# Kernel tuning notes

Hardware: AMD Instinct MI355X
Metric: run time of the kernel (lower is better)

## Reference

```python
import jax, jax.numpy as jnp
import numpy as np

K = 256            # number of learned permutations (config['k'])
N = 256            # nb_experts
NOISE_FACTOR = 0.01
TAU_INITIAL = 1e-3
TAU_FINAL = 1e-7
N_ITERS_MIN, N_ITERS_MAX = 20, 150
ITERS_TOTAL = 100 * 1000   # epochs_for_learning_permutation * steps_per_epoch
EPS = 1e-20


def setup_inputs() -> dict:
    key = jax.random.key(0)
    k1, k2 = jax.random.split(key)
    # keras RandomUniform initializer default range is [-0.05, 0.05]
    plw = jax.random.uniform(k1, (K, N, N), jnp.float32, minval=-0.05, maxval=0.05)
    u = jax.random.uniform(k2, (K, N, N), jnp.float32)
    return {"permutation_log_weights": plw, "u": u, "iterations": 5000}


def reference(permutation_log_weights, u, iterations):
    # Linear-in-log10 interpolation of tau and linear interpolation of n_iters
    # over the learning schedule (tfp.math.interp_regular_1d_grid with clamping).
    frac = min(max(float(iterations) / ITERS_TOTAL, 0.0), 1.0)
    log_tau = np.log10(TAU_INITIAL) + frac * (np.log10(TAU_FINAL) - np.log10(TAU_INITIAL))
    tau = np.float32(10.0 ** log_tau)
    n_iters = int(N_ITERS_MIN + frac * (N_ITERS_MAX - N_ITERS_MIN))

    # Gumbel noise from uniform samples, scaled, then temperature scaling.
    noise = -jnp.log(-jnp.log(u + EPS) + EPS) * jnp.float32(NOISE_FACTOR)
    log_alpha = (permutation_log_weights + noise) / tau  # [K, N, N]

    # Log-domain Sinkhorn: alternate row / column log-normalization.
    def step(la, _):
        la = la - jax.scipy.special.logsumexp(la, axis=2, keepdims=True)
        la = la - jax.scipy.special.logsumexp(la, axis=1, keepdims=True)
        return la, None

    log_alpha, _ = jax.lax.scan(step, log_alpha, None, length=n_iters)
    return jnp.exp(log_alpha)  # [K, N, N] near-doubly-stochastic
```

## Files before the change

kernel.cpp:

```cpp
#include <hip/hip_runtime.h>


#define KMAT 256

typedef unsigned uint2_ev __attribute__((ext_vector_type(2)));

__device__ __forceinline__ float fast_exp2(float x) {
#if __has_builtin(__builtin_amdgcn_exp2f)
  return __builtin_amdgcn_exp2f(x);
#else
  return exp2f(x);
#endif
}

__device__ __forceinline__ float fast_log2(float x) {
#if __has_builtin(__builtin_amdgcn_logf)
  return __builtin_amdgcn_logf(x);
#else
  return __log2f(x);
#endif
}

__device__ __forceinline__ float fast_rcp(float x) {
#if __has_builtin(__builtin_amdgcn_rcpf)
  return __builtin_amdgcn_rcpf(x);
#else
  return 1.0f / x;
#endif
}

__device__ __forceinline__ float2 pk_fma(float2 a, float2 b, float2 c) {
  float2 d;
  asm("v_pk_fma_f32 %0, %1, %2, %3" : "=v"(d) : "v"(a), "v"(b), "v"(c));
  return d;
}
__device__ __forceinline__ float2 pk_mul(float2 a, float2 b) {
  float2 d;
  asm("v_pk_mul_f32 %0, %1, %2" : "=v"(d) : "v"(a), "v"(b));
  return d;
}
__device__ __forceinline__ float2 pk_add(float2 a, float2 b) {
  float2 d;
  asm("v_pk_add_f32 %0, %1, %2" : "=v"(d) : "v"(a), "v"(b));
  return d;
}
__device__ __forceinline__ float2 pk_sub1(float2 a, float s) {
  return make_float2(a.x - s, a.y - s);
}

template <int CTRL>
__device__ __forceinline__ float dpp_movf(float x) {
  return __int_as_float(
      __builtin_amdgcn_update_dpp(0, __float_as_int(x), CTRL, 0xf, 0xf, true));
}

__device__ __forceinline__ float hgroup_max(float x) {
  x = fmaxf(x, dpp_movf<0x121>(x));
  x = fmaxf(x, dpp_movf<0x122>(x));
  x = fmaxf(x, dpp_movf<0x124>(x));
  x = fmaxf(x, dpp_movf<0x128>(x));
#if __has_builtin(__builtin_amdgcn_permlane16_swap)
  uint2_ev r = __builtin_amdgcn_permlane16_swap(
      (unsigned)__float_as_int(x), (unsigned)__float_as_int(x), false, false);
  return fmaxf(__int_as_float((int)r.x), __int_as_float((int)r.y));
#else
  return fmaxf(x, __shfl_xor(x, 16, 64));
#endif
}

__device__ __forceinline__ float hgroup_sum(float x) {
  x += dpp_movf<0x121>(x);
  x += dpp_movf<0x122>(x);
  x += dpp_movf<0x124>(x);
  x += dpp_movf<0x128>(x);
#if __has_builtin(__builtin_amdgcn_permlane16_swap)
  uint2_ev r = __builtin_amdgcn_permlane16_swap(
      (unsigned)__float_as_int(x), (unsigned)__float_as_int(x), false, false);
  return __int_as_float((int)r.x) + __int_as_float((int)r.y);
#else
  return x + __shfl_xor(x, 16, 64);
#endif
}

__device__ __forceinline__ float x32_max(float x) {
#if __has_builtin(__builtin_amdgcn_permlane32_swap)
  uint2_ev r = __builtin_amdgcn_permlane32_swap(
      (unsigned)__float_as_int(x), (unsigned)__float_as_int(x), false, false);
  return fmaxf(__int_as_float((int)r.x), __int_as_float((int)r.y));
#else
  return fmaxf(x, __shfl_xor(x, 32, 64));
#endif
}

__device__ __forceinline__ float x32_sum(float x) {
#if __has_builtin(__builtin_amdgcn_permlane32_swap)
  uint2_ev r = __builtin_amdgcn_permlane32_swap(
      (unsigned)__float_as_int(x), (unsigned)__float_as_int(x), false, false);
  return __int_as_float((int)r.x) + __int_as_float((int)r.y);
#else
  return x + __shfl_xor(x, 32, 64);
#endif
}

__device__ __forceinline__ float gumbel_la(float p, float uv, float scale) {
  float lnu = fast_log2(uv + 1e-20f) * 0.69314718056f;
  float g = fast_log2(1e-20f - lnu) * (-0.0069314718056f);
  return (p + g) * scale;
}

__global__ __launch_bounds__(1024, 4) void lp_sinkhorn_kernel(
    const float* __restrict__ plw, const float* __restrict__ uin,
    const int* __restrict__ itp, float* __restrict__ out) {
  const int k = blockIdx.x;
  const int t = threadIdx.x;
  const int br = t >> 5;
  const int bc = t & 31;
  const int wv = t >> 6;
  const int lane = t & 63;

  __shared__ float red[16 * 256];
  __shared__ float colv[256];

  double frac = (double)itp[0] * 1e-5;
  frac = frac < 0.0 ? 0.0 : (frac > 1.0 ? 1.0 : frac);
  const int n_iters = (int)(20.0 + frac * 130.0);
  const float tauf = (float)exp2((-3.0 - 4.0 * frac) * 3.3219280948873623);
  const float scale = (float)(1.4426950408889634 / (double)tauf);

  float2 la[8][4];

  const float4* p4 = (const float4*)plw + k * 16384;
  const float4* u4 = (const float4*)uin + k * 16384;
#pragma unroll
  for (int i = 0; i < 8; ++i) {
    const int ridx = ((br << 3) + i) * 64 + (bc << 1);
    float4 p0 = p4[ridx];
    float4 p1 = p4[ridx + 1];
    float4 v0 = u4[ridx];
    float4 v1 = u4[ridx + 1];
    la[i][0] = make_float2(gumbel_la(p0.x, v0.x, scale),
                           gumbel_la(p0.y, v0.y, scale));
    la[i][1] = make_float2(gumbel_la(p0.z, v0.z, scale),
                           gumbel_la(p0.w, v0.w, scale));
    la[i][2] = make_float2(gumbel_la(p1.x, v1.x, scale),
                           gumbel_la(p1.y, v1.y, scale));
    la[i][3] = make_float2(gumbel_la(p1.z, v1.z, scale),
                           gumbel_la(p1.w, v1.w, scale));
  }

  const int jlo = (lane < 32) ? 0 : 4;

#pragma unroll
  for (int i = 0; i < 8; ++i) {
    float m = fmaxf(la[i][0].x, la[i][0].y);
#pragma unroll
    for (int p = 1; p < 4; ++p) m = fmaxf(m, fmaxf(la[i][p].x, la[i][p].y));
    m = hgroup_max(m);
    float s = 0.f;
#pragma unroll
    for (int p = 0; p < 4; ++p)
      s += fast_exp2(la[i][p].x - m) + fast_exp2(la[i][p].y - m);
    s = hgroup_sum(s);
    const float lse = m + fast_log2(s);
#pragma unroll
    for (int p = 0; p < 4; ++p) la[i][p] = pk_sub1(la[i][p], lse);
  }

  {
    float cm[8];
#pragma unroll
    for (int p = 0; p < 4; ++p) {
      float2 m = la[0][p];
#pragma unroll
      for (int i = 1; i < 8; ++i)
        m = make_float2(fmaxf(m.x, la[i][p].x), fmaxf(m.y, la[i][p].y));
      cm[2 * p] = x32_max(m.x);
      cm[2 * p + 1] = x32_max(m.y);
    }
#pragma unroll
    for (int j = 0; j < 4; ++j) red[wv * 256 + bc + 32 * (jlo + j)] = cm[jlo + j];
    __syncthreads();

    float keepm = 0.f;
    if (t < 256) {
      float v = red[t];
#pragma unroll
      for (int w = 1; w < 16; ++w) v = fmaxf(v, red[w * 256 + t]);
      keepm = v;
      colv[t] = v;
    }
    __syncthreads();

    float cs[8];
#pragma unroll
    for (int p = 0; p < 4; ++p) {
      const float2 mj = make_float2(colv[bc + 32 * (2 * p)],
                                    colv[bc + 32 * (2 * p + 1)]);
      float2 s = make_float2(0.f, 0.f);
#pragma unroll
      for (int i = 0; i < 8; ++i)
        s = make_float2(s.x + fast_exp2(la[i][p].x - mj.x),
                        s.y + fast_exp2(la[i][p].y - mj.y));
      cs[2 * p] = x32_sum(s.x);
      cs[2 * p + 1] = x32_sum(s.y);
    }
    __syncthreads();
#pragma unroll
    for (int j = 0; j < 4; ++j) red[wv * 256 + bc + 32 * (jlo + j)] = cs[jlo + j];
    __syncthreads();

    if (t < 256) {
      float v = red[t];
#pragma unroll
      for (int w = 1; w < 16; ++w) v += red[w * 256 + t];
      colv[t] = keepm + fast_log2(v);
    }
    __syncthreads();

#pragma unroll
    for (int p = 0; p < 4; ++p) {
      const float2 lse = make_float2(colv[bc + 32 * (2 * p)],
                                     colv[bc + 32 * (2 * p + 1)]);
#pragma unroll
      for (int i = 0; i < 8; ++i)
        la[i][p] = make_float2(fast_exp2(la[i][p].x - lse.x),
                               fast_exp2(la[i][p].y - lse.y));
    }
  }

  float uo[8] = {1.f, 1.f, 1.f, 1.f, 1.f, 1.f, 1.f, 1.f};
  float2 v2[4] = {make_float2(1.f, 1.f), make_float2(1.f, 1.f),
                  make_float2(1.f, 1.f), make_float2(1.f, 1.f)};

  for (int iter = 1; iter < n_iters; ++iter) {
#pragma unroll
    for (int i = 0; i < 8; ++i) {
      float2 a0 = pk_mul(la[i][0], v2[0]);
      float2 a1 = pk_mul(la[i][1], v2[1]);
      a0 = pk_fma(la[i][2], v2[2], a0);
      a1 = pk_fma(la[i][3], v2[3], a1);
      a0 = pk_add(a0, a1);
      const float s = hgroup_sum(a0.x + a0.y);
      uo[i] = fast_rcp(s);
    }

    float2 cs2[4] = {make_float2(0.f, 0.f), make_float2(0.f, 0.f),
                     make_float2(0.f, 0.f), make_float2(0.f, 0.f)};
#pragma unroll
    for (int i = 0; i < 8; ++i) {
      const float2 ub = make_float2(uo[i], uo[i]);
#pragma unroll
      for (int p = 0; p < 4; ++p) cs2[p] = pk_fma(la[i][p], ub, cs2[p]);
    }
    float cs[8];
#pragma unroll
    for (int p = 0; p < 4; ++p) {
      cs[2 * p] = x32_sum(cs2[p].x);
      cs[2 * p + 1] = x32_sum(cs2[p].y);
    }
#pragma unroll
    for (int j = 0; j < 4; ++j) red[wv * 256 + bc + 32 * (jlo + j)] = cs[jlo + j];
    __syncthreads();

    if (t < 128) {
      const float2* r2 = (const float2*)red;
      float2 v = r2[t];
#pragma unroll
      for (int w = 1; w < 16; ++w) v = pk_add(v, r2[w * 128 + t]);
      float2* c2 = (float2*)colv;
      c2[t] = make_float2(fast_rcp(v.x), fast_rcp(v.y));
    }
    __syncthreads();

#pragma unroll
    for (int p = 0; p < 4; ++p)
      v2[p] = make_float2(colv[bc + 32 * (2 * p)],
                          colv[bc + 32 * (2 * p + 1)]);
  }

  float4* o4 = (float4*)out + k * 16384;
#pragma unroll
  for (int i = 0; i < 8; ++i) {
    const int ridx = ((br << 3) + i) * 64 + (bc << 1);
    const float2 ub = make_float2(uo[i], uo[i]);
    float2 r0 = pk_mul(pk_mul(la[i][0], ub), v2[0]);
    float2 r1 = pk_mul(pk_mul(la[i][1], ub), v2[1]);
    float2 r2 = pk_mul(pk_mul(la[i][2], ub), v2[2]);
    float2 r3 = pk_mul(pk_mul(la[i][3], ub), v2[3]);
    float4 a, b;
    a.x = r0.x; a.y = r0.y; a.z = r1.x; a.w = r1.y;
    b.x = r2.x; b.y = r2.y; b.z = r3.x; b.w = r3.y;
    o4[ridx] = a;
    o4[ridx + 1] = b;
  }
}

extern "C" void kernel_launch(void* const* d_in, const int* in_sizes, int n_in,
                              void* d_out, int out_size, void* d_ws,
                              size_t ws_size, hipStream_t stream) {
  const float* plw = (const float*)d_in[0];
  const float* u = (const float*)d_in[1];
  const int* iters = (const int*)d_in[2];
  float* out = (float*)d_out;
  (void)in_sizes; (void)n_in; (void)out_size; (void)d_ws; (void)ws_size;
  lp_sinkhorn_kernel<<<dim3(KMAT), dim3(1024), 0, stream>>>(plw, u, iters, out);
}
```

Before: 99.97 us.

## Replace cross-half permlane32 column reduction with padded LDS all-thread reduction

Column partial sums and maxes are no longer combined across wave halves with permlane32 swaps. Every thread now writes its per-column partials into a larger padded LDS buffer, one row per 32-thread group. All 1024 threads then reduce it, four lanes per column, finishing with DPP quad shuffles instead of 128 or 256 threads doing serial 16-way loops. The inline-asm packed FP32 helpers are replaced with scalar float code the compiler can schedule, and the launch bounds move to an explicit waves-per-EU attribute. The aim is a shorter critical path in the per-iteration column reduction, at the cost of more LDS traffic and possibly losing packed-math issue.

```diff
diff --git a/kernel.cpp b/kernel.cpp
--- a/kernel.cpp
+++ b/kernel.cpp
@@ -2,6 +2,7 @@
 
 
 #define KMAT 256
+#define RSTRIDE 264
 
 typedef unsigned uint2_ev __attribute__((ext_vector_type(2)));
 
@@ -27,25 +28,6 @@
 #else
   return 1.0f / x;
 #endif
-}
-
-__device__ __forceinline__ float2 pk_fma(float2 a, float2 b, float2 c) {
-  float2 d;
-  asm("v_pk_fma_f32 %0, %1, %2, %3" : "=v"(d) : "v"(a), "v"(b), "v"(c));
-  return d;
-}
-__device__ __forceinline__ float2 pk_mul(float2 a, float2 b) {
-  float2 d;
-  asm("v_pk_mul_f32 %0, %1, %2" : "=v"(d) : "v"(a), "v"(b));
-  return d;
-}
-__device__ __forceinline__ float2 pk_add(float2 a, float2 b) {
-  float2 d;
-  asm("v_pk_add_f32 %0, %1, %2" : "=v"(d) : "v"(a), "v"(b));
-  return d;
-}
-__device__ __forceinline__ float2 pk_sub1(float2 a, float s) {
-  return make_float2(a.x - s, a.y - s);
 }
 
 template <int CTRL>
@@ -82,33 +64,15 @@
 #endif
 }
 
-__device__ __forceinline__ float x32_max(float x) {
-#if __has_builtin(__builtin_amdgcn_permlane32_swap)
-  uint2_ev r = __builtin_amdgcn_permlane32_swap(
-      (unsigned)__float_as_int(x), (unsigned)__float_as_int(x), false, false);
-  return fmaxf(__int_as_float((int)r.x), __int_as_float((int)r.y));
-#else
-  return fmaxf(x, __shfl_xor(x, 32, 64));
-#endif
-}
-
-__device__ __forceinline__ float x32_sum(float x) {
-#if __has_builtin(__builtin_amdgcn_permlane32_swap)
-  uint2_ev r = __builtin_amdgcn_permlane32_swap(
-      (unsigned)__float_as_int(x), (unsigned)__float_as_int(x), false, false);
-  return __int_as_float((int)r.x) + __int_as_float((int)r.y);
-#else
-  return x + __shfl_xor(x, 32, 64);
-#endif
-}
-
 __device__ __forceinline__ float gumbel_la(float p, float uv, float scale) {
   float lnu = fast_log2(uv + 1e-20f) * 0.69314718056f;
   float g = fast_log2(1e-20f - lnu) * (-0.0069314718056f);
   return (p + g) * scale;
 }
 
-__global__ __launch_bounds__(1024, 4) void lp_sinkhorn_kernel(
+__global__ __launch_bounds__(1024)
+__attribute__((amdgpu_waves_per_eu(4, 4)))
+void lp_sinkhorn_kernel(
     const float* __restrict__ plw, const float* __restrict__ uin,
     const int* __restrict__ itp, float* __restrict__ out) {
   const int k = blockIdx.x;
@@ -118,8 +82,12 @@
   const int wv = t >> 6;
   const int lane = t & 63;
 
-  __shared__ float red[16 * 256];
+  __shared__ float red[32 * RSTRIDE];
   __shared__ float colv[256];
+
+  const int rbase = br * RSTRIDE + bc;
+  const int slot = 16 * wv + (lane >> 2);
+  const int q = lane & 3;
 
   double frac = (double)itp[0] * 1e-5;
   frac = frac < 0.0 ? 0.0 : (frac > 1.0 ? 1.0 : frac);
@@ -148,8 +116,6 @@
                            gumbel_la(p1.w, v1.w, scale));
   }
 
-  const int jlo = (lane < 32) ? 0 : 4;
-
 #pragma unroll
   for (int i = 0; i < 8; ++i) {
     float m = fmaxf(la[i][0].x, la[i][0].y);
@@ -163,35 +129,33 @@
     s = hgroup_sum(s);
     const float lse = m + fast_log2(s);
 #pragma unroll
-    for (int p = 0; p < 4; ++p) la[i][p] = pk_sub1(la[i][p], lse);
+    for (int p = 0; p < 4; ++p)
+      la[i][p] = make_float2(la[i][p].x - lse, la[i][p].y - lse);
   }
 
   {
-    float cm[8];
 #pragma unroll
     for (int p = 0; p < 4; ++p) {
       float2 m = la[0][p];
 #pragma unroll
       for (int i = 1; i < 8; ++i)
         m = make_float2(fmaxf(m.x, la[i][p].x), fmaxf(m.y, la[i][p].y));
-      cm[2 * p] = x32_max(m.x);
-      cm[2 * p + 1] = x32_max(m.y);
-    }
-#pragma unroll
-    for (int j = 0; j < 4; ++j) red[wv * 256 + bc + 32 * (jlo + j)] = cm[jlo + j];
-    __syncthreads();
-
-    float keepm = 0.f;
-    if (t < 256) {
-      float v = red[t];
-#pragma unroll
-      for (int w = 1; w < 16; ++w) v = fmaxf(v, red[w * 256 + t]);
-      keepm = v;
-      colv[t] = v;
-    }
-    __syncthreads();
-
-    float cs[8];
+      red[rbase + 32 * (2 * p)] = m.x;
+      red[rbase + 32 * (2 * p + 1)] = m.y;
+    }
+    __syncthreads();
+
+    {
+      float v = red[q * RSTRIDE + slot];
+#pragma unroll
+      for (int m = 1; m < 8; ++m)
+        v = fmaxf(v, red[(q + 4 * m) * RSTRIDE + slot]);
+      v = fmaxf(v, dpp_movf<0xB1>(v));
+      v = fmaxf(v, dpp_movf<0x4E>(v));
+      if (q == 0) colv[slot] = v;
+    }
+    __syncthreads();
+
 #pragma unroll
     for (int p = 0; p < 4; ++p) {
       const float2 mj = make_float2(colv[bc + 32 * (2 * p)],
@@ -201,19 +165,19 @@
       for (int i = 0; i < 8; ++i)
         s = make_float2(s.x + fast_exp2(la[i][p].x - mj.x),
                         s.y + fast_exp2(la[i][p].y - mj.y));
-      cs[2 * p] = x32_sum(s.x);
-      cs[2 * p + 1] = x32_sum(s.y);
-    }
-    __syncthreads();
-#pragma unroll
-    for (int j = 0; j < 4; ++j) red[wv * 256 + bc + 32 * (jlo + j)] = cs[jlo + j];
-    __syncthreads();
-
-    if (t < 256) {
-      float v = red[t];
-#pragma unroll
-      for (int w = 1; w < 16; ++w) v += red[w * 256 + t];
-      colv[t] = keepm + fast_log2(v);
+      red[rbase + 32 * (2 * p)] = s.x;
+      red[rbase + 32 * (2 * p + 1)] = s.y;
+    }
+    __syncthreads();
+
+    {
+      float v = red[q * RSTRIDE + slot];
+#pragma unroll
+      for (int m = 1; m < 8; ++m) v += red[(q + 4 * m) * RSTRIDE + slot];
+      v += dpp_movf<0xB1>(v);
+      v += dpp_movf<0x4E>(v);
+      const float lse = colv[slot] + fast_log2(v);
+      if (q == 0) colv[slot] = lse;
     }
     __syncthreads();
 
@@ -235,12 +199,13 @@
   for (int iter = 1; iter < n_iters; ++iter) {
 #pragma unroll
     for (int i = 0; i < 8; ++i) {
-      float2 a0 = pk_mul(la[i][0], v2[0]);
-      float2 a1 = pk_mul(la[i][1], v2[1]);
-      a0 = pk_fma(la[i][2], v2[2], a0);
-      a1 = pk_fma(la[i][3], v2[3], a1);
-      a0 = pk_add(a0, a1);
-      const float s = hgroup_sum(a0.x + a0.y);
+      float2 a0 = make_float2(la[i][0].x * v2[0].x, la[i][0].y * v2[0].y);
+      float2 a1 = make_float2(la[i][1].x * v2[1].x, la[i][1].y * v2[1].y);
+      a0 = make_float2(fmaf(la[i][2].x, v2[2].x, a0.x),
+                       fmaf(la[i][2].y, v2[2].y, a0.y));
+      a1 = make_float2(fmaf(la[i][3].x, v2[3].x, a1.x),
+                       fmaf(la[i][3].y, v2[3].y, a1.y));
+      const float s = hgroup_sum((a0.x + a1.x) + (a0.y + a1.y));
       uo[i] = fast_rcp(s);
     }
 
@@ -248,27 +213,26 @@
                      make_float2(0.f, 0.f), make_float2(0.f, 0.f)};
 #pragma unroll
     for (int i = 0; i < 8; ++i) {
-      const float2 ub = make_float2(uo[i], uo[i]);
-#pragma unroll
-      for (int p = 0; p < 4; ++p) cs2[p] = pk_fma(la[i][p], ub, cs2[p]);
-    }
-    float cs[8];
-#pragma unroll
-    for (int p = 0; p < 4; ++p) {
-      cs[2 * p] = x32_sum(cs2[p].x);
-      cs[2 * p + 1] = x32_sum(cs2[p].y);
-    }
-#pragma unroll
-    for (int j = 0; j < 4; ++j) red[wv * 256 + bc + 32 * (jlo + j)] = cs[jlo + j];
-    __syncthreads();
-
-    if (t < 128) {
-      const float2* r2 = (const float2*)red;
-      float2 v = r2[t];
-#pragma unroll
-      for (int w = 1; w < 16; ++w) v = pk_add(v, r2[w * 128 + t]);
-      float2* c2 = (float2*)colv;
-      c2[t] = make_float2(fast_rcp(v.x), fast_rcp(v.y));
+      const float u = uo[i];
+#pragma unroll
+      for (int p = 0; p < 4; ++p)
+        cs2[p] = make_float2(fmaf(la[i][p].x, u, cs2[p].x),
+                             fmaf(la[i][p].y, u, cs2[p].y));
+    }
+#pragma unroll
+    for (int p = 0; p < 4; ++p) {
+      red[rbase + 32 * (2 * p)] = cs2[p].x;
+      red[rbase + 32 * (2 * p + 1)] = cs2[p].y;
+    }
+    __syncthreads();
+
+    {
+      float v = red[q * RSTRIDE + slot];
+#pragma unroll
+      for (int m = 1; m < 8; ++m) v += red[(q + 4 * m) * RSTRIDE + slot];
+      v += dpp_movf<0xB1>(v);
+      v += dpp_movf<0x4E>(v);
+      if (q == 0) colv[slot] = fast_rcp(v);
     }
     __syncthreads();
 
@@ -282,14 +246,16 @@
 #pragma unroll
   for (int i = 0; i < 8; ++i) {
     const int ridx = ((br << 3) + i) * 64 + (bc << 1);
-    const float2 ub = make_float2(uo[i], uo[i]);
-    float2 r0 = pk_mul(pk_mul(la[i][0], ub), v2[0]);
-    float2 r1 = pk_mul(pk_mul(la[i][1], ub), v2[1]);
-    float2 r2 = pk_mul(pk_mul(la[i][2], ub), v2[2]);
-    float2 r3 = pk_mul(pk_mul(la[i][3], ub), v2[3]);
+    const float u = uo[i];
     float4 a, b;
-    a.x = r0.x; a.y = r0.y; a.z = r1.x; a.w = r1.y;
-    b.x = r2.x; b.y = r2.y; b.z = r3.x; b.w = r3.y;
+    a.x = la[i][0].x * u * v2[0].x;
+    a.y = la[i][0].y * u * v2[0].y;
+    a.z = la[i][1].x * u * v2[1].x;
+    a.w = la[i][1].y * u * v2[1].y;
+    b.x = la[i][2].x * u * v2[2].x;
+    b.y = la[i][2].y * u * v2[2].y;
+    b.z = la[i][3].x * u * v2[3].x;
+    b.w = la[i][3].y * u * v2[3].y;
     o4[ridx] = a;
     o4[ridx + 1] = b;
   }
```

Measured after the change: 91.32 us. 1.09x faster.
